# Performance work log

Measured on AMD Instinct MI355X. Metric: run time of the kernel, lower is better.

Reference implementation:

```python
import jax, jax.numpy as jnp
import numpy as np

N = 50000   # nodes
E = 600000  # edges
D = 128     # input_dim
H = 128     # hidden_dim
K = 2       # num_layers (propagation hops)


def setup_inputs() -> dict:
    key = jax.random.key(0)
    k1, k2, k3 = jax.random.split(key, 3)
    x = jax.random.normal(k1, (N, D), dtype=jnp.float32)
    edge_index = jax.random.randint(k2, (2, E), 0, N, dtype=jnp.int64)
    # Linear(input_dim -> hidden_dim) params (PyG default: glorot-ish weight, zero bias)
    W = jax.random.normal(k3, (H, D), dtype=jnp.float32) / np.float32(np.sqrt(D))
    b = jnp.zeros((H,), dtype=jnp.float32)
    return {"x": x, "edge_index": edge_index, "W": W, "b": b}


def reference(x, edge_index, W, b):
    n = x.shape[0]
    loop = jnp.arange(n, dtype=edge_index.dtype)
    # gcn_norm: add self-loops with weight 1, symmetric normalization
    row = jnp.concatenate([edge_index[0], loop])  # source nodes
    col = jnp.concatenate([edge_index[1], loop])  # target nodes
    w = jnp.ones(row.shape[0], dtype=x.dtype)
    deg = jax.ops.segment_sum(w, col, num_segments=n)
    dinv = jnp.where(deg > 0, jax.lax.rsqrt(deg), jnp.zeros_like(deg))
    norm = dinv[row] * w * dinv[col]  # [E+N]
    # K hops of normalized sparse propagation: x <- A_hat @ x
    for _ in range(K):
        x = jax.ops.segment_sum(norm[:, None] * x[row], col, num_segments=n)
    # Linear projection + activation
    z = x @ W.T + b
    return jax.nn.relu(z)
```

## Files before the change

kernel.cpp:

```cpp
#include <hip/hip_runtime.h>

#define D 128
#define CAP 128
#define NR 8
typedef unsigned int uint;
typedef unsigned short ushort;
typedef __attribute__((ext_vector_type(8))) short bf16x8;
typedef __attribute__((ext_vector_type(4))) float f32x4;

__device__ __forceinline__ float2 bf2_to_f2(uint v) {
    union { uint u; float f; } a, b;
    a.u = v << 16;
    b.u = v & 0xffff0000u;
    return make_float2(a.f, b.f);
}
__device__ __forceinline__ uint f2_to_bf2(float x, float y) {
    uint xu = __float_as_uint(x), yu = __float_as_uint(y);
    xu += 0x7fffu + ((xu >> 16) & 1u);
    yu += 0x7fffu + ((yu >> 16) & 1u);
    return (xu >> 16) | (yu & 0xffff0000u);
}

__global__ __launch_bounds__(256) void edge_build_kernel(
        const int* __restrict__ ei, int E, int n,
        int* __restrict__ deg, int* __restrict__ slots,
        const float* __restrict__ W, uint* __restrict__ Wbf, int edgeB) {
    int b = blockIdx.x, t = threadIdx.x;
    if (b < edgeB) {
        int range = b & (NR - 1);
        int e = (b >> 3) * 256 + t;
        if (e < E) {
            int c = ei[E + e];
            int per = (n + NR - 1) / NR;
            int lo = range * per;
            if (c >= lo && c < lo + per) {
                int r = ei[e];
                int pos = atomicAdd(&deg[c], 1);
                if (pos < CAP) slots[(size_t)c * CAP + pos] = r;
            }
        }
    } else {
        int i = (b - edgeB) * 256 + t;
        if (i < (D * D) / 2) {
            float2 wv = ((const float2*)W)[i];
            Wbf[i] = f2_to_bf2(wv.x, wv.y);
        }
    }
}

__global__ __launch_bounds__(256) void scale_cast_kernel(
        const float* __restrict__ x, const int* __restrict__ deg,
        uint2* __restrict__ zX, int n) {
    int idx = blockIdx.x * 256 + threadIdx.x;
    if (idx < n * 32) {
        int node = idx >> 5;
        float dv = rsqrtf((float)(deg[node] + 1));
        float4 v = ((const float4*)x)[idx];
        uint2 o;
        o.x = f2_to_bf2(v.x * dv, v.y * dv);
        o.y = f2_to_bf2(v.z * dv, v.w * dv);
        zX[idx] = o;
    }
}

template<bool HOP1>
__global__ __launch_bounds__(256) void prop_kernel(const uint* __restrict__ zin,
                                                   uint* __restrict__ zout,
                                                   const int* __restrict__ deg,
                                                   const int* __restrict__ slots,
                                                   int n) {
    int wv = threadIdx.x >> 6, lane = threadIdx.x & 63;
    int c = blockIdx.x * 4 + wv;
    if (c >= n) return;
    int len = deg[c]; if (len > CAP) len = CAP;
    const int* lst = slots + (size_t)c * CAP;
    size_t selfoff = (size_t)c * 64 + lane;
    float2 acc = bf2_to_f2(zin[selfoff]);
    int k = 0;
    for (; k + 7 < len; k += 8) {
        int r0 = lst[k],     r1 = lst[k + 1], r2 = lst[k + 2], r3 = lst[k + 3];
        int r4 = lst[k + 4], r5 = lst[k + 5], r6 = lst[k + 6], r7 = lst[k + 7];
        uint v0 = zin[(size_t)r0 * 64 + lane], v1 = zin[(size_t)r1 * 64 + lane];
        uint v2 = zin[(size_t)r2 * 64 + lane], v3 = zin[(size_t)r3 * 64 + lane];
        uint v4 = zin[(size_t)r4 * 64 + lane], v5 = zin[(size_t)r5 * 64 + lane];
        uint v6 = zin[(size_t)r6 * 64 + lane], v7 = zin[(size_t)r7 * 64 + lane];
        float2 f0 = bf2_to_f2(v0), f1 = bf2_to_f2(v1), f2 = bf2_to_f2(v2), f3 = bf2_to_f2(v3);
        float2 f4 = bf2_to_f2(v4), f5 = bf2_to_f2(v5), f6 = bf2_to_f2(v6), f7 = bf2_to_f2(v7);
        acc.x += ((f0.x + f1.x) + (f2.x + f3.x)) + ((f4.x + f5.x) + (f6.x + f7.x));
        acc.y += ((f0.y + f1.y) + (f2.y + f3.y)) + ((f4.y + f5.y) + (f6.y + f7.y));
    }
    if (k + 3 < len) {
        int r0 = lst[k], r1 = lst[k + 1], r2 = lst[k + 2], r3 = lst[k + 3];
        uint v0 = zin[(size_t)r0 * 64 + lane], v1 = zin[(size_t)r1 * 64 + lane];
        uint v2 = zin[(size_t)r2 * 64 + lane], v3 = zin[(size_t)r3 * 64 + lane];
        float2 f0 = bf2_to_f2(v0), f1 = bf2_to_f2(v1), f2 = bf2_to_f2(v2), f3 = bf2_to_f2(v3);
        acc.x += (f0.x + f1.x) + (f2.x + f3.x);
        acc.y += (f0.y + f1.y) + (f2.y + f3.y);
        k += 4;
    }
    if (k + 1 < len) {
        int r0 = lst[k], r1 = lst[k + 1];
        uint v0 = zin[(size_t)r0 * 64 + lane], v1 = zin[(size_t)r1 * 64 + lane];
        float2 f0 = bf2_to_f2(v0), f1 = bf2_to_f2(v1);
        acc.x += f0.x + f1.x;
        acc.y += f0.y + f1.y;
        k += 2;
    }
    if (k < len) {
        float2 f = bf2_to_f2(zin[(size_t)lst[k] * 64 + lane]);
        acc.x += f.x; acc.y += f.y;
    }
    float s = rsqrtf((float)(len + 1));
    float sc = HOP1 ? s * s : s;
    zout[selfoff] = f2_to_bf2(acc.x * sc, acc.y * sc);
}

#define GN 64
__global__ __launch_bounds__(256) void gemm_mfma(const uint4* __restrict__ x2,
                                                 const uint4* __restrict__ Wbf,
                                                 const float* __restrict__ bias,
                                                 float* __restrict__ out, int n) {
    __shared__ __align__(16) ushort xs[GN][136];
    __shared__ __align__(16) ushort ws[D][136];
    int t = threadIdx.x;
    int n0 = blockIdx.x * GN;
    for (int i = t; i < D * 16; i += 256) {
        int row = i >> 4, c8 = i & 15;
        uint4 v = Wbf[i];
        *(uint4*)&ws[row][c8 * 8] = v;
    }
    for (int i = t; i < GN * 16; i += 256) {
        int row = i >> 4, c8 = i & 15;
        int node = n0 + row;
        uint4 v = (node < n) ? x2[(size_t)node * 16 + c8] : make_uint4(0u, 0u, 0u, 0u);
        *(uint4*)&xs[row][c8 * 8] = v;
    }
    __syncthreads();

    int w = t >> 6, lane = t & 63;
    int m0 = w * 16;
    int mrow = lane & 15, quad = lane >> 4;

    bf16x8 a[4];
#pragma unroll
    for (int q = 0; q < 4; ++q)
        a[q] = *(const bf16x8*)&xs[m0 + mrow][q * 32 + quad * 8];

    f32x4 acc[8];
#pragma unroll
    for (int ht = 0; ht < 8; ++ht) {
        acc[ht] = (f32x4){0.f, 0.f, 0.f, 0.f};
#pragma unroll
        for (int q = 0; q < 4; ++q) {
            bf16x8 bfr = *(const bf16x8*)&ws[ht * 16 + mrow][q * 32 + quad * 8];
            acc[ht] = __builtin_amdgcn_mfma_f32_16x16x32_bf16(a[q], bfr, acc[ht], 0, 0, 0);
        }
    }

#pragma unroll
    for (int ht = 0; ht < 8; ++ht) {
        int h = ht * 16 + mrow;
        float bv = bias[h];
#pragma unroll
        for (int reg = 0; reg < 4; ++reg) {
            int node = n0 + m0 + quad * 4 + reg;
            if (node < n)
                out[(size_t)node * D + h] = fmaxf(acc[ht][reg] + bv, 0.f);
        }
    }
}

extern "C" void kernel_launch(void* const* d_in, const int* in_sizes, int n_in,
                              void* d_out, int out_size, void* d_ws, size_t ws_size,
                              hipStream_t stream) {
    const float* x  = (const float*)d_in[0];
    const int*   ei = (const int*)d_in[1];
    const float* W  = (const float*)d_in[2];
    const float* bias = (const float*)d_in[3];
    float* out = (float*)d_out;
    int N = in_sizes[0] / D;
    int E = in_sizes[1] / 2;

    char* p = (char*)d_ws;
    auto alloc = [&](size_t bytes) -> void* {
        void* r = p; p += (bytes + 511) & ~(size_t)511; return r;
    };
    int*    deg     = (int*)alloc((size_t)N * 4);
    int*    slots   = (int*)alloc((size_t)N * CAP * 4);
    uint*   zX      = (uint*)alloc((size_t)N * 64 * 4);
    uint*   zB      = (uint*)alloc((size_t)N * 64 * 4);
    uint*   zA      = (uint*)alloc((size_t)N * 64 * 4);
    uint*   Wbf     = (uint*)alloc((size_t)(D * D / 2) * 4);

    int edgeB = ((E + 255) / 256) * NR;
    int wB    = ((D * D / 2) + 255) / 256;
    int xB    = (N * 32 + 255) / 256;

    hipMemsetAsync(deg, 0, (size_t)N * 4, stream);
    edge_build_kernel<<<edgeB + wB, 256, 0, stream>>>(ei, E, N, deg, slots, W, Wbf, edgeB);
    scale_cast_kernel<<<xB, 256, 0, stream>>>(x, deg, (uint2*)zX, N);
    prop_kernel<true ><<<(N + 3) / 4, 256, 0, stream>>>(zX, zB, deg, slots, N);
    prop_kernel<false><<<(N + 3) / 4, 256, 0, stream>>>(zB, zA, deg, slots, N);
    gemm_mfma<<<(N + GN - 1) / GN, 256, 0, stream>>>((const uint4*)zA, (const uint4*)Wbf, bias, out, N);
}
```

Baseline: 180.0 us.

## Fuse second propagation hop into MFMA GEMM via per-wave LDS tiles

```diff
diff --git a/kernel.cpp b/kernel.cpp
--- a/kernel.cpp
+++ b/kernel.cpp
@@ -19,6 +19,44 @@
     xu += 0x7fffu + ((xu >> 16) & 1u);
     yu += 0x7fffu + ((yu >> 16) & 1u);
     return (xu >> 16) | (yu & 0xffff0000u);
+}
+
+__device__ __forceinline__ void sum8(const uint* __restrict__ zin, const int* __restrict__ lst,
+                                     int k, int lane, float2& acc) {
+    int r0 = lst[k],     r1 = lst[k + 1], r2 = lst[k + 2], r3 = lst[k + 3];
+    int r4 = lst[k + 4], r5 = lst[k + 5], r6 = lst[k + 6], r7 = lst[k + 7];
+    uint v0 = zin[(size_t)r0 * 64 + lane], v1 = zin[(size_t)r1 * 64 + lane];
+    uint v2 = zin[(size_t)r2 * 64 + lane], v3 = zin[(size_t)r3 * 64 + lane];
+    uint v4 = zin[(size_t)r4 * 64 + lane], v5 = zin[(size_t)r5 * 64 + lane];
+    uint v6 = zin[(size_t)r6 * 64 + lane], v7 = zin[(size_t)r7 * 64 + lane];
+    float2 f0 = bf2_to_f2(v0), f1 = bf2_to_f2(v1), f2 = bf2_to_f2(v2), f3 = bf2_to_f2(v3);
+    float2 f4 = bf2_to_f2(v4), f5 = bf2_to_f2(v5), f6 = bf2_to_f2(v6), f7 = bf2_to_f2(v7);
+    acc.x += ((f0.x + f1.x) + (f2.x + f3.x)) + ((f4.x + f5.x) + (f6.x + f7.x));
+    acc.y += ((f0.y + f1.y) + (f2.y + f3.y)) + ((f4.y + f5.y) + (f6.y + f7.y));
+}
+__device__ __forceinline__ void sum4(const uint* __restrict__ zin, const int* __restrict__ lst,
+                                     int k, int lane, float2& acc) {
+    int r0 = lst[k], r1 = lst[k + 1], r2 = lst[k + 2], r3 = lst[k + 3];
+    uint v0 = zin[(size_t)r0 * 64 + lane], v1 = zin[(size_t)r1 * 64 + lane];
+    uint v2 = zin[(size_t)r2 * 64 + lane], v3 = zin[(size_t)r3 * 64 + lane];
+    float2 f0 = bf2_to_f2(v0), f1 = bf2_to_f2(v1), f2 = bf2_to_f2(v2), f3 = bf2_to_f2(v3);
+    acc.x += (f0.x + f1.x) + (f2.x + f3.x);
+    acc.y += (f0.y + f1.y) + (f2.y + f3.y);
+}
+__device__ __forceinline__ void tail2_1(const uint* __restrict__ zin, const int* __restrict__ lst,
+                                        int& k, int len, int lane, float2& acc) {
+    if (k + 1 < len) {
+        int r0 = lst[k], r1 = lst[k + 1];
+        uint v0 = zin[(size_t)r0 * 64 + lane], v1 = zin[(size_t)r1 * 64 + lane];
+        float2 f0 = bf2_to_f2(v0), f1 = bf2_to_f2(v1);
+        acc.x += f0.x + f1.x;
+        acc.y += f0.y + f1.y;
+        k += 2;
+    }
+    if (k < len) {
+        float2 f = bf2_to_f2(zin[(size_t)lst[k] * 64 + lane]);
+        acc.x += f.x; acc.y += f.y;
+    }
 }
 
 __global__ __launch_bounds__(256) void edge_build_kernel(
@@ -63,12 +101,11 @@
     }
 }
 
-template<bool HOP1>
-__global__ __launch_bounds__(256) void prop_kernel(const uint* __restrict__ zin,
-                                                   uint* __restrict__ zout,
-                                                   const int* __restrict__ deg,
-                                                   const int* __restrict__ slots,
-                                                   int n) {
+__global__ __launch_bounds__(256) void prop1_kernel(const uint* __restrict__ zin,
+                                                    uint* __restrict__ zout,
+                                                    const int* __restrict__ deg,
+                                                    const int* __restrict__ slots,
+                                                    int n) {
     int wv = threadIdx.x >> 6, lane = threadIdx.x & 63;
     int c = blockIdx.x * 4 + wv;
     if (c >= n) return;
@@ -77,69 +114,63 @@
     size_t selfoff = (size_t)c * 64 + lane;
     float2 acc = bf2_to_f2(zin[selfoff]);
     int k = 0;
-    for (; k + 7 < len; k += 8) {
-        int r0 = lst[k],     r1 = lst[k + 1], r2 = lst[k + 2], r3 = lst[k + 3];
-        int r4 = lst[k + 4], r5 = lst[k + 5], r6 = lst[k + 6], r7 = lst[k + 7];
-        uint v0 = zin[(size_t)r0 * 64 + lane], v1 = zin[(size_t)r1 * 64 + lane];
-        uint v2 = zin[(size_t)r2 * 64 + lane], v3 = zin[(size_t)r3 * 64 + lane];
-        uint v4 = zin[(size_t)r4 * 64 + lane], v5 = zin[(size_t)r5 * 64 + lane];
-        uint v6 = zin[(size_t)r6 * 64 + lane], v7 = zin[(size_t)r7 * 64 + lane];
-        float2 f0 = bf2_to_f2(v0), f1 = bf2_to_f2(v1), f2 = bf2_to_f2(v2), f3 = bf2_to_f2(v3);
-        float2 f4 = bf2_to_f2(v4), f5 = bf2_to_f2(v5), f6 = bf2_to_f2(v6), f7 = bf2_to_f2(v7);
-        acc.x += ((f0.x + f1.x) + (f2.x + f3.x)) + ((f4.x + f5.x) + (f6.x + f7.x));
-        acc.y += ((f0.y + f1.y) + (f2.y + f3.y)) + ((f4.y + f5.y) + (f6.y + f7.y));
-    }
-    if (k + 3 < len) {
-        int r0 = lst[k], r1 = lst[k + 1], r2 = lst[k + 2], r3 = lst[k + 3];
-        uint v0 = zin[(size_t)r0 * 64 + lane], v1 = zin[(size_t)r1 * 64 + lane];
-        uint v2 = zin[(size_t)r2 * 64 + lane], v3 = zin[(size_t)r3 * 64 + lane];
-        float2 f0 = bf2_to_f2(v0), f1 = bf2_to_f2(v1), f2 = bf2_to_f2(v2), f3 = bf2_to_f2(v3);
-        acc.x += (f0.x + f1.x) + (f2.x + f3.x);
-        acc.y += (f0.y + f1.y) + (f2.y + f3.y);
-        k += 4;
-    }
-    if (k + 1 < len) {
-        int r0 = lst[k], r1 = lst[k + 1];
-        uint v0 = zin[(size_t)r0 * 64 + lane], v1 = zin[(size_t)r1 * 64 + lane];
-        float2 f0 = bf2_to_f2(v0), f1 = bf2_to_f2(v1);
-        acc.x += f0.x + f1.x;
-        acc.y += f0.y + f1.y;
-        k += 2;
-    }
-    if (k < len) {
-        float2 f = bf2_to_f2(zin[(size_t)lst[k] * 64 + lane]);
-        acc.x += f.x; acc.y += f.y;
-    }
+    for (; k + 7 < len; k += 8) sum8(zin, lst, k, lane, acc);
+    if (k + 3 < len) { sum4(zin, lst, k, lane, acc); k += 4; }
+    tail2_1(zin, lst, k, len, lane, acc);
     float s = rsqrtf((float)(len + 1));
-    float sc = HOP1 ? s * s : s;
+    float sc = s * s;
     zout[selfoff] = f2_to_bf2(acc.x * sc, acc.y * sc);
 }
 
-#define GN 64
-__global__ __launch_bounds__(256) void gemm_mfma(const uint4* __restrict__ x2,
-                                                 const uint4* __restrict__ Wbf,
-                                                 const float* __restrict__ bias,
-                                                 float* __restrict__ out, int n) {
+#define GN 32
+__global__ __launch_bounds__(128) void prop2_gemm(const uint* __restrict__ zin,
+                                                  const int* __restrict__ deg,
+                                                  const int* __restrict__ slots,
+                                                  const uint4* __restrict__ Wbf4,
+                                                  const float* __restrict__ bias,
+                                                  float* __restrict__ out, int n) {
     __shared__ __align__(16) ushort xs[GN][136];
-    __shared__ __align__(16) ushort ws[D][136];
     int t = threadIdx.x;
-    int n0 = blockIdx.x * GN;
-    for (int i = t; i < D * 16; i += 256) {
-        int row = i >> 4, c8 = i & 15;
-        uint4 v = Wbf[i];
-        *(uint4*)&ws[row][c8 * 8] = v;
-    }
-    for (int i = t; i < GN * 16; i += 256) {
-        int row = i >> 4, c8 = i & 15;
-        int node = n0 + row;
-        uint4 v = (node < n) ? x2[(size_t)node * 16 + c8] : make_uint4(0u, 0u, 0u, 0u);
-        *(uint4*)&xs[row][c8 * 8] = v;
-    }
-    __syncthreads();
-
-    int w = t >> 6, lane = t & 63;
-    int m0 = w * 16;
+    int wv = t >> 6, lane = t & 63;
+    int base = blockIdx.x * GN + wv * 16;
+
+    for (int i = 0; i < 16; i += 2) {
+        int cA = base + i, cB = base + i + 1;
+        bool vA = cA < n, vB = cB < n;
+        int lenA = 0, lenB = 0;
+        if (vA) { lenA = deg[cA]; if (lenA > CAP) lenA = CAP; }
+        if (vB) { lenB = deg[cB]; if (lenB > CAP) lenB = CAP; }
+        const int* lstA = slots + (size_t)cA * CAP;
+        const int* lstB = slots + (size_t)cB * CAP;
+        float2 accA = make_float2(0.f, 0.f), accB = make_float2(0.f, 0.f);
+        if (vA) accA = bf2_to_f2(zin[(size_t)cA * 64 + lane]);
+        if (vB) accB = bf2_to_f2(zin[(size_t)cB * 64 + lane]);
+        int kA = 0, kB = 0;
+        while (kA + 7 < lenA && kB + 7 < lenB) {
+            sum8(zin, lstA, kA, lane, accA);
+            sum8(zin, lstB, kB, lane, accB);
+            kA += 8; kB += 8;
+        }
+        for (; kA + 7 < lenA; kA += 8) sum8(zin, lstA, kA, lane, accA);
+        for (; kB + 7 < lenB; kB += 8) sum8(zin, lstB, kB, lane, accB);
+        if (kA + 3 < lenA) { sum4(zin, lstA, kA, lane, accA); kA += 4; }
+        if (kB + 3 < lenB) { sum4(zin, lstB, kB, lane, accB); kB += 4; }
+        tail2_1(zin, lstA, kA, lenA, lane, accA);
+        tail2_1(zin, lstB, kB, lenB, lane, accB);
+        if (vA) {
+            float s = rsqrtf((float)(lenA + 1));
+            *(uint*)&xs[wv * 16 + i][lane * 2] = f2_to_bf2(accA.x * s, accA.y * s);
+        }
+        if (vB) {
+            float s = rsqrtf((float)(lenB + 1));
+            *(uint*)&xs[wv * 16 + i + 1][lane * 2] = f2_to_bf2(accB.x * s, accB.y * s);
+        }
+    }
+    asm volatile("s_waitcnt lgkmcnt(0)" ::: "memory");
+    __builtin_amdgcn_sched_barrier(0);
+
     int mrow = lane & 15, quad = lane >> 4;
+    int m0 = wv * 16;
 
     bf16x8 a[4];
 #pragma unroll
@@ -152,8 +183,9 @@
         acc[ht] = (f32x4){0.f, 0.f, 0.f, 0.f};
 #pragma unroll
         for (int q = 0; q < 4; ++q) {
-            bf16x8 bfr = *(const bf16x8*)&ws[ht * 16 + mrow][q * 32 + quad * 8];
-            acc[ht] = __builtin_amdgcn_mfma_f32_16x16x32_bf16(a[q], bfr, acc[ht], 0, 0, 0);
+            uint4 bv = Wbf4[(ht * 16 + mrow) * 16 + q * 4 + quad];
+            union { uint4 u; bf16x8 b; } cvt; cvt.u = bv;
+            acc[ht] = __builtin_amdgcn_mfma_f32_16x16x32_bf16(a[q], cvt.b, acc[ht], 0, 0, 0);
         }
     }
 
@@ -163,7 +195,7 @@
         float bv = bias[h];
 #pragma unroll
         for (int reg = 0; reg < 4; ++reg) {
-            int node = n0 + m0 + quad * 4 + reg;
+            int node = base + quad * 4 + reg;
             if (node < n)
                 out[(size_t)node * D + h] = fmaxf(acc[ht][reg] + bv, 0.f);
         }
@@ -189,7 +221,6 @@
     int*    slots   = (int*)alloc((size_t)N * CAP * 4);
     uint*   zX      = (uint*)alloc((size_t)N * 64 * 4);
     uint*   zB      = (uint*)alloc((size_t)N * 64 * 4);
-    uint*   zA      = (uint*)alloc((size_t)N * 64 * 4);
     uint*   Wbf     = (uint*)alloc((size_t)(D * D / 2) * 4);
 
     int edgeB = ((E + 255) / 256) * NR;
@@ -199,7 +230,6 @@
     hipMemsetAsync(deg, 0, (size_t)N * 4, stream);
     edge_build_kernel<<<edgeB + wB, 256, 0, stream>>>(ei, E, N, deg, slots, W, Wbf, edgeB);
     scale_cast_kernel<<<xB, 256, 0, stream>>>(x, deg, (uint2*)zX, N);
-    prop_kernel<true ><<<(N + 3) / 4, 256, 0, stream>>>(zX, zB, deg, slots, N);
-    prop_kernel<false><<<(N + 3) / 4, 256, 0, stream>>>(zB, zA, deg, slots, N);
-    gemm_mfma<<<(N + GN - 1) / GN, 256, 0, stream>>>((const uint4*)zA, (const uint4*)Wbf, bias, out, N);
-}
+    prop1_kernel<<<(N + 3) / 4, 256, 0, stream>>>(zX, zB, deg, slots, N);
+    prop2_gemm<<<(N + GN - 1) / GN, 128, 0, stream>>>(zB, deg, slots, (const uint4*)Wbf, bias, out, N);
+}
```

Result: slower. 193.3 us (+7.4%).
